# Optimization experiments

Measured on AMD Instinct MI355X. Metric: run time of the kernel, lower is better.

The kernel has to match this reference:

```python
import jax, jax.numpy as jnp
import numpy as np

# Qwen3.5-MoE Gated DeltaNet dims (from module defaults)
H = 16       # num v/k/q heads
DK = 128     # key head dim
DV = 128     # value head dim
HID = 3072   # hidden size
KD = H * DK  # key_dim = 2048
VD = H * DV  # value_dim = 2048
CONV_DIM = 2 * KD + VD  # 6144
KW = 4       # conv kernel width
EPS = 1e-6


def setup_inputs() -> dict:
    key = jax.random.key(0)
    ks = jax.random.split(key, 9)
    return {
        "hidden_states": jax.random.normal(ks[0], (2, 4096, HID), jnp.float32),
        "W_qkvz": jax.random.normal(ks[1], (HID, 2 * KD + 2 * VD), jnp.float32) * 0.02,
        "W_ba": jax.random.normal(ks[2], (HID, 2 * H), jnp.float32) * 0.02,
        "conv_w": jax.random.normal(ks[3], (CONV_DIM, KW), jnp.float32) * 0.1,
        "conv_b": jax.random.normal(ks[4], (CONV_DIM,), jnp.float32) * 0.01,
        "dt_bias": jax.random.normal(ks[5], (H,), jnp.float32) * 0.1,
        "A_log": jax.random.normal(ks[6], (H,), jnp.float32) * 0.1,
        "norm_w": jnp.ones((DV,), jnp.float32),
        "W_out": jax.random.normal(ks[7], (VD, HID), jnp.float32) * 0.02,
    }


def _l2norm(x):
    return x * jax.lax.rsqrt(jnp.sum(x * x, axis=-1, keepdims=True) + EPS)


def _gated_delta_net(hidden_states, W_qkvz, W_ba, conv_w, conv_b,
                     dt_bias, A_log, norm_w, W_out):
    B, T, _ = hidden_states.shape

    # unified qkvz projection, split [KD, KD, VD, VD]
    qkvz = hidden_states @ W_qkvz                       # [B,T,2KD+2VD]
    mixed_qkv = qkvz[..., :2 * KD + VD]                 # q|k|v  [B,T,CONV_DIM]
    z = qkvz[..., 2 * KD + VD:]                         # [B,T,VD]

    # causal depthwise conv1d over time + silu
    rhs = conv_w.T[:, None, :]                          # [KW,1,C]
    conv_out = jax.lax.conv_general_dilated(
        mixed_qkv, rhs, window_strides=(1,), padding=[(KW - 1, 0)],
        dimension_numbers=("NWC", "WIO", "NWC"),
        feature_group_count=CONV_DIM)
    mixed_qkv = jax.nn.silu(conv_out + conv_b)

    q = mixed_qkv[..., :KD].reshape(B, T, H, DK)
    k = mixed_qkv[..., KD:2 * KD].reshape(B, T, H, DK)
    v = mixed_qkv[..., 2 * KD:].reshape(B, T, H, DV)

    # beta / gate projections
    ba = hidden_states @ W_ba                           # [B,T,2H]
    beta = jax.nn.sigmoid(ba[..., :H])                  # [B,T,H]
    a = ba[..., H:]
    g = -jnp.exp(A_log) * jax.nn.softplus(a + dt_bias)  # [B,T,H] log-decay

    q = _l2norm(q) * (DK ** -0.5)
    k = _l2norm(k)

    # gated delta-rule recurrence over time (time-major scan)
    def step(S, inp):
        q_t, k_t, v_t, g_t, b_t = inp                   # [B,H,*]
        S = S * jnp.exp(g_t)[..., None, None]           # decay state [B,H,DK,DV]
        kv = jnp.einsum("bhk,bhkv->bhv", k_t, S)
        delta = (v_t - kv) * b_t[..., None]
        S = S + jnp.einsum("bhk,bhv->bhkv", k_t, delta)
        o_t = jnp.einsum("bhk,bhkv->bhv", q_t, S)
        return S, o_t

    tm = lambda x: jnp.moveaxis(x, 1, 0)                # [T,B,H,*]
    S0 = jnp.zeros((B, H, DK, DV), hidden_states.dtype)
    S_fin, o = jax.lax.scan(step, S0, (tm(q), tm(k), tm(v), tm(g), tm(beta)))
    o = jnp.moveaxis(o, 0, 1)                           # [B,T,H,DV]

    # gated RMSNorm (gate applied before norm, Mamba2/Qwen3-Next style)
    gate = jax.nn.silu(z.reshape(B, T, H, DV))
    x = o * gate
    x = x * jax.lax.rsqrt(jnp.mean(x * x, axis=-1, keepdims=True) + EPS) * norm_w

    out = x.reshape(B, T, VD) @ W_out                   # [B,T,HID]
    return out


def reference(hidden_states, W_qkvz, W_ba, conv_w, conv_b,
              dt_bias, A_log, norm_w, W_out):
    return _gated_delta_net(hidden_states, W_qkvz, W_ba, conv_w, conv_b,
                            dt_bias, A_log, norm_w, W_out)
```

## Files before the change

kernel.cpp:

```cpp
#include <hip/hip_runtime.h>
#include <cstdint>
#include <cstddef>

#define T_SEQ 4096
#define HID 3072
#define NH 16
#define DKH 128
#define KD 2048
#define VD 2048
#define N_QKVZ 8192
#define CONV_CH 6144
#define MROWS 8192

typedef unsigned short u16;
typedef unsigned int u32;

typedef __attribute__((ext_vector_type(8))) short bf16x8;
typedef __attribute__((ext_vector_type(4))) float f32x4;

__device__ __forceinline__ float bf2f(u16 u){ u32 t=((u32)u)<<16; float f; __builtin_memcpy(&f,&t,4); return f; }
__device__ __forceinline__ float bflo(u32 u){ u32 t=u<<16; float f; __builtin_memcpy(&f,&t,4); return f; }
__device__ __forceinline__ float bfhi(u32 u){ u32 t=u&0xffff0000u; float f; __builtin_memcpy(&f,&t,4); return f; }
__device__ __forceinline__ u16 f2bf(float f){ u32 i; __builtin_memcpy(&i,&f,4); return (u16)((i + 0x7fffu + ((i>>16)&1u))>>16); }

__device__ __forceinline__ void gl_lds16(const u16* g, u16* l){
    __builtin_amdgcn_global_load_lds(
        (const __attribute__((address_space(1))) void*)g,
        (__attribute__((address_space(3))) void*)l, 16, 0, 0);
}

__device__ __forceinline__ bf16x8 frag(const u16* p, int row, int stride, int k0){
    return *(const bf16x8*)(p + (size_t)row*stride + k0);
}

__global__ void k_cast(const float* __restrict__ in, u16* __restrict__ out, int n4){
    int stride = gridDim.x*blockDim.x;
    for (int i = blockIdx.x*blockDim.x + threadIdx.x; i < n4; i += stride){
        float4 v = ((const float4*)in)[i];
        u32 lo = (u32)f2bf(v.x) | ((u32)f2bf(v.y)<<16);
        u32 hi = (u32)f2bf(v.z) | ((u32)f2bf(v.w)<<16);
        ((uint2*)out)[i] = make_uint2(lo,hi);
    }
}

__global__ void k_transpose_cast(const float* __restrict__ in, u16* __restrict__ out, int R, int C){
    __shared__ u16 tile[32][33];
    int nbc = C >> 5;
    int bc = blockIdx.x % nbc, br = blockIdx.x / nbc;
    int c0 = bc<<5, r0 = br<<5;
    int tx = threadIdx.x & 31, ty = threadIdx.x >> 5;
    #pragma unroll
    for (int i=0;i<4;i++){
        int r = ty + i*8;
        tile[r][tx] = f2bf(in[(size_t)(r0+r)*C + c0 + tx]);
    }
    __syncthreads();
    #pragma unroll
    for (int i=0;i<4;i++){
        int r = ty + i*8;
        out[(size_t)(c0+r)*R + r0 + tx] = tile[tx][r];
    }
}

template<bool OUT_BF16>
__global__ __launch_bounds__(256, 2) void k_gemm_bt(const u16* __restrict__ A, const u16* __restrict__ Bt,
                                                 void* __restrict__ C1, void* __restrict__ C2,
                                                 int M, int N, int K, int csplit, int ld1, int ld2){
    __shared__ __align__(16) u16 SM[4*128*64];
    u16 (*As)[128*64] = (u16(*)[128*64])SM;
    u16 (*Bs)[128*64] = (u16(*)[128*64])(SM + 2*128*64);
    const int tid  = threadIdx.x;
    const int lane = tid & 63;
    const int wave = tid >> 6;
    const int wm = (wave >> 1) << 6;
    const int wn = (wave & 1) << 6;
    const int lr = lane & 15, lg = lane >> 4;
    const int nbn = N >> 7;
    const int per = 8*nbn;
    const int grp = blockIdx.x / per, rem = blockIdx.x % per;
    const int bm = grp*8 + (rem & 7);
    const int bn = rem >> 3;
    f32x4 acc[4][4] = {};
    const size_t aRow0 = (size_t)bm*128;
    const size_t bRow0 = (size_t)bn*128;
    const int srow = wave*32 + (lane>>3);
    const int scol = (lane&7)*8;

    auto STAGE = [&](int kt, int b){
        const u16* ga = A  + (aRow0 + srow)*K + kt + scol;
        const u16* gb = Bt + (bRow0 + srow)*K + kt + scol;
        u16* la = &As[b][wave*2048];
        u16* lb = &Bs[b][wave*2048];
        #pragma unroll
        for (int i=0;i<4;i++){
            gl_lds16(ga + (size_t)i*8*K, la + i*512);
            gl_lds16(gb + (size_t)i*8*K, lb + i*512);
        }
    };

    STAGE(0, 0);
    __syncthreads();

    const int NT = K >> 6;
    int cur = 0;
    for (int t = 0; t < NT; t++){
        if (t+1 < NT) STAGE((t+1)*64, cur^1);
        #pragma unroll
        for (int kk=0; kk<2; kk++){
            bf16x8 af[4], bfv[4];
            #pragma unroll
            for (int i=0;i<4;i++){
                af[i]  = *(const bf16x8*)&As[cur][((wm + i*16 + lr)<<6) + (kk<<5) + (lg<<3)];
                bfv[i] = *(const bf16x8*)&Bs[cur][((wn + i*16 + lr)<<6) + (kk<<5) + (lg<<3)];
            }
            __builtin_amdgcn_s_setprio(1);
            #pragma unroll
            for (int i=0;i<4;i++)
                #pragma unroll
                for (int j=0;j<4;j++)
                    acc[i][j] = __builtin_amdgcn_mfma_f32_16x16x32_bf16(af[i], bfv[j], acc[i][j], 0, 0, 0);
            __builtin_amdgcn_s_setprio(0);
        }
        __syncthreads();
        cur ^= 1;
    }

    if (OUT_BF16){
        u16* Cs = SM;
        #pragma unroll
        for (int i=0;i<4;i++)
            #pragma unroll
            for (int j=0;j<4;j++)
                #pragma unroll
                for (int r=0;r<4;r++)
                    Cs[(wm + i*16 + lg*4 + r)*136 + wn + j*16 + lr] = f2bf(acc[i][j][r]);
        __syncthreads();
        int row = tid >> 1, half = tid & 1;
        int colbase = bn*128 + half*64;
        u16* dst; int ld;
        if (bn*128 < csplit){ dst = (u16*)C1; ld = ld1; }
        else { dst = (u16*)C2; ld = ld2; colbase -= csplit; }
        u16* gp = dst + (size_t)(bm*128+row)*ld + colbase;
        const u16* sp = Cs + row*136 + half*64;
        #pragma unroll
        for (int k2=0;k2<8;k2++) *(uint4*)(gp + k2*8) = *(const uint4*)(sp + k2*8);
    } else {
        #pragma unroll
        for (int i=0;i<4;i++)
            #pragma unroll
            for (int j=0;j<4;j++)
                #pragma unroll
                for (int r=0;r<4;r++){
                    int row = bm*128 + wm + i*16 + lg*4 + r;
                    int col = bn*128 + wn + j*16 + lr;
                    ((float*)C1)[(size_t)row*ld1 + col] = acc[i][j][r];
                }
    }
}

__global__ void k_ba(const float* __restrict__ hidden, const float* __restrict__ W_ba,
                     const float* __restrict__ dt_bias, const float* __restrict__ A_log,
                     float2* __restrict__ be){
    int row = blockIdx.x*8 + (threadIdx.x>>5);
    int col = threadIdx.x & 31;
    const float* h = hidden + (size_t)row*HID;
    float s0=0.f, s1=0.f, s2=0.f, s3=0.f;
    #pragma unroll 2
    for (int k=0;k<HID;k+=4){
        s0 = fmaf(h[k],   W_ba[(k)*32+col],   s0);
        s1 = fmaf(h[k+1], W_ba[(k+1)*32+col], s1);
        s2 = fmaf(h[k+2], W_ba[(k+2)*32+col], s2);
        s3 = fmaf(h[k+3], W_ba[(k+3)*32+col], s3);
    }
    float s = (s0+s1)+(s2+s3);
    if (col < NH){
        be[(size_t)row*NH + col].x = 1.f/(1.f+expf(-s));
    } else {
        int hh = col - NH;
        float x = s + dt_bias[hh];
        float sp = fmaxf(x,0.f) + log1pf(expf(-fabsf(x)));
        be[(size_t)row*NH + hh].y = -expf(A_log[hh])*sp;
    }
}

__global__ __launch_bounds__(256) void k_conv_silu(const u16* __restrict__ qkv, const float* __restrict__ conv_w,
                            const float* __restrict__ conv_b, u16* __restrict__ mixed){
    __shared__ float hsum[4][8];
    const int bid = blockIdx.x, tid = threadIdx.x;
    const int c0 = (bid % 24) << 8;
    const long bt0 = (long)(bid / 24) * 8;
    const int ts0 = (int)(bt0 % T_SEQ);
    const int c = c0 + tid;
    const u16* in = qkv + (size_t)bt0*CONV_CH + c;
    float4 w = *(const float4*)(conv_w + c*4);
    float bias = conv_b[c];
    float w0=0.f, w1=0.f, w2=0.f;
    if (ts0 > 0){
        w0 = bf2f(in[-3*CONV_CH]); w1 = bf2f(in[-2*CONV_CH]); w2 = bf2f(in[-1*CONV_CH]);
    }
    float sv[8];
    #pragma unroll
    for (int j=0;j<8;j++){
        float xc = bf2f(in[(ptrdiff_t)j*CONV_CH]);
        float acc = bias + w.x*w0 + w.y*w1 + w.z*w2 + w.w*xc;
        sv[j] = acc / (1.f + __expf(-acc));
        w0 = w1; w1 = w2; w2 = xc;
    }
    if (c0 < 2*KD){
        float ss[8];
        #pragma unroll
        for (int j=0;j<8;j++) ss[j] = sv[j]*sv[j];
        #pragma unroll
        for (int m=1;m<64;m<<=1)
            #pragma unroll
            for (int j=0;j<8;j++) ss[j] += __shfl_xor(ss[j], m, 64);
        if ((tid&63)==0)
            #pragma unroll
            for (int j=0;j<8;j++) hsum[tid>>6][j] = ss[j];
        __syncthreads();
        int head = tid>>7;
        float qs = (c0 + head*128 < KD) ? 0.08838834764831845f : 1.f;
        #pragma unroll
        for (int j=0;j<8;j++){
            float tot = hsum[head*2][j] + hsum[head*2+1][j];
            sv[j] *= rsqrtf(tot + 1e-6f) * qs;
        }
    }
    u16* outp = mixed + (size_t)bt0*CONV_CH + c;
    #pragma unroll
    for (int j=0;j<8;j++) outp[(size_t)j*CONV_CH] = f2bf(sv[j]);
}

__global__ __launch_bounds__(512) void k_prep(const u16* __restrict__ mixed,
        const float2* __restrict__ be, u16* __restrict__ Wcg, u16* __restrict__ Ucg,
        float* __restrict__ barr){
    __shared__ __align__(16) u16 Ks[64*128];
    __shared__ __align__(16) u16 Vs[64*128];
    __shared__ float Am[64*64];
    __shared__ __align__(16) float RHS[64*256];
    __shared__ float bv[64], betav[64], lamv[64];
    const int tid = threadIdx.x;
    const int lane = tid & 63, wave = tid >> 6;
    const int lr = lane & 15, lg = lane >> 4;
    const int chunk = blockIdx.x;
    const int ci = chunk & 63, bh = chunk >> 6, b = bh >> 4, h = bh & 15;
    const size_t rowbase = (size_t)b*T_SEQ + ci*64;

    const u16* kg = mixed + rowbase*CONV_CH + KD + h*128;
    const u16* vg = mixed + rowbase*CONV_CH + 2*KD + h*128;
    #pragma unroll
    for (int pass=0; pass<2; pass++){
        int row = (tid>>4) + pass*32;
        int co = (tid&15)*8;
        gl_lds16(kg + (size_t)row*CONV_CH + co, Ks + row*128 + co);
        gl_lds16(vg + (size_t)row*CONV_CH + co, Vs + row*128 + co);
    }
    if (tid < 64){
        float2 bg = be[(rowbase + tid)*NH + h];
        float acc = bg.y;
        #pragma unroll
        for (int m=1;m<64;m<<=1){ float u = __shfl_up(acc, m, 64); if (tid >= m) acc += u; }
        bv[tid] = acc; betav[tid] = bg.x; lamv[tid] = __expf(acc);
        barr[(size_t)chunk*64 + tid] = acc;
    }
    __syncthreads();
    #pragma unroll
    for (int i=0;i<2;i++){
        int tile = wave*2 + i;
        int tm = tile>>2, tn = tile&3;
        f32x4 acc = {};
        #pragma unroll
        for (int kk=0;kk<4;kk++)
            acc = __builtin_amdgcn_mfma_f32_16x16x32_bf16(
                frag(Ks, tm*16+lr, 128, kk*32+lg*8),
                frag(Ks, tn*16+lr, 128, kk*32+lg*8), acc, 0,0,0);
        #pragma unroll
        for (int r=0;r<4;r++){
            int t = tm*16 + lg*4 + r, s = tn*16 + lr;
            Am[t*64+s] = (t>s) ? betav[t]*__expf(bv[t]-bv[s])*acc[r] : 0.f;
        }
    }
    __syncthreads();
    for (int i=tid; i<64*256; i+=512){
        int r = i>>8, j = i&255;
        RHS[i] = (j<128) ? betav[r]*lamv[r]*bf2f(Ks[r*128+j])
                         : betav[r]*bf2f(Vs[r*128 + (j-128)]);
    }
    __syncthreads();
    for (int blk=0; blk<8; blk++){
        int base = blk*8;
        if (base){
            int r = base + (tid>>6);
            int j0 = (tid&63)*4;
            float4 x = *(float4*)&RHS[r*256 + j0];
            for (int s=0; s<base; s++){
                float a = Am[r*64+s];
                float4 y = *(float4*)&RHS[s*256 + j0];
                x.x = fmaf(-a, y.x, x.x); x.y = fmaf(-a, y.y, x.y);
                x.z = fmaf(-a, y.z, x.z); x.w = fmaf(-a, y.w, x.w);
            }
            *(float4*)&RHS[r*256 + j0] = x;
        }
        __syncthreads();
        if (tid < 256){
            float x[8];
            #pragma unroll
            for (int i=0;i<8;i++) x[i] = RHS[(base+i)*256 + tid];
            #pragma unroll
            for (int r=1;r<8;r++)
                #pragma unroll
                for (int s=0;s<r;s++)
                    x[r] = fmaf(-Am[(base+r)*64 + base+s], x[s], x[r]);
            #pragma unroll
            for (int i=1;i<8;i++) RHS[(base+i)*256 + tid] = x[i];
        }
        __syncthreads();
    }
    for (int i=tid; i<8192; i+=512){
        int r = i>>7, c = i&127;
        Wcg[(size_t)chunk*8192 + i] = f2bf(RHS[r*256 + c]);
        Ucg[(size_t)chunk*8192 + i] = f2bf(RHS[r*256 + 128 + c]);
    }
}

__global__ __launch_bounds__(256) void k_seq(const u16* __restrict__ mixed,
        const u16* __restrict__ Wcg, const u16* __restrict__ Ucg,
        const float* __restrict__ barr,
        float* __restrict__ o1g, u16* __restrict__ DTg){
    __shared__ __align__(16) u16 WcS[2][64*128];
    __shared__ __align__(16) u16 Ks[2][64*128];
    __shared__ __align__(16) u16 Qs[2][64*128];
    __shared__ __align__(16) u16 UcS[2][64*32];
    __shared__ __align__(16) u16 KpT[128*72];
    __shared__ __align__(16) u16 DT[32*72];
    __shared__ __align__(16) u16 STh[32*136];
    __shared__ __align__(16) u16 STl[32*136];
    __shared__ float bvv[2][64], esc[64];
    const int tid = threadIdx.x, lane = tid&63, wave = tid>>6;
    const int lr = lane&15, lg = lane>>4;
    const int blk = blockIdx.x;
    const int bh = blk & 31, vs = blk >> 5;
    const int b = bh>>4, h = bh&15, v0 = vs*32;
    const u16* qgb = mixed + (size_t)b*T_SEQ*CONV_CH + h*128;
    const u16* kgb = qgb + KD;
    const int urow = tid>>2, uc8 = (tid&3)*8;

    float sreg[4][4];
    #pragma unroll
    for (int i=0;i<4;i++)
        #pragma unroll
        for (int r=0;r<4;r++) sreg[i][r] = 0.f;
    for (int i=tid; i<32*136; i+=256){ STh[i]=0; STl[i]=0; }

    auto STAGE = [&](int ci2, int bf){
        const size_t ch = (size_t)(bh*64 + ci2);
        #pragma unroll
        for (int pass=0; pass<4; pass++){
            gl_lds16(Wcg + ch*8192 + pass*2048 + tid*8, &WcS[bf][pass*2048 + tid*8]);
            int row = pass*16 + (tid>>4), co = (tid&15)*8;
            gl_lds16(kgb + ((size_t)(ci2*64) + row)*CONV_CH + co, &Ks[bf][row*128 + co]);
            gl_lds16(qgb + ((size_t)(ci2*64) + row)*CONV_CH + co, &Qs[bf][row*128 + co]);
        }
    };

    STAGE(0, 0);
    *(uint4*)&UcS[0][urow*32 + uc8] = *(const uint4*)(Ucg + (size_t)(bh*64)*8192 + urow*128 + v0 + uc8);
    if (tid<64) bvv[0][tid] = barr[(size_t)(bh*64)*64 + tid];
    __syncthreads();

    for (int ci=0; ci<64; ci++){
        const int cur = ci&1, nxt = cur^1;
        const size_t chunk = (size_t)(bh*64 + ci);
        const size_t rowbase = (size_t)b*T_SEQ + ci*64;
        uint4 ucv = {0,0,0,0}; float bvn = 0.f;
        const bool havenext = (ci+1 < 64);
        if (havenext){
            STAGE(ci+1, nxt);
            ucv = *(const uint4*)(Ucg + (chunk+1)*8192 + urow*128 + v0 + uc8);
            if (tid<64) bvn = barr[(chunk+1)*64 + tid];
        }
        if (tid<64) esc[tid] = __expf(bvv[cur][63] - bvv[cur][tid]);
        #pragma unroll
        for (int i=0;i<2;i++){
            int tile = wave*2 + i, tm = tile>>1, tn = tile&1;
            f32x4 acc = {};
            #pragma unroll
            for (int kk=0;kk<4;kk++){
                bf16x8 af = frag(WcS[cur], tm*16+lr, 128, kk*32+lg*8);
                acc = __builtin_amdgcn_mfma_f32_16x16x32_bf16(af, frag(STh, tn*16+lr, 136, kk*32+lg*8), acc, 0,0,0);
                acc = __builtin_amdgcn_mfma_f32_16x16x32_bf16(af, frag(STl, tn*16+lr, 136, kk*32+lg*8), acc, 0,0,0);
            }
            #pragma unroll
            for (int r=0;r<4;r++){
                int t = tm*16+lg*4+r, vv = tn*16+lr;
                DT[vv*72 + t] = f2bf(bf2f(UcS[cur][t*32+vv]) - acc[r]);
            }
        }
        #pragma unroll
        for (int i=0;i<2;i++){
            int tile = wave*2 + i, tm = tile>>1, tn = tile&1;
            f32x4 acc = {};
            #pragma unroll
            for (int kk=0;kk<4;kk++){
                bf16x8 af = frag(Qs[cur], tm*16+lr, 128, kk*32+lg*8);
                acc = __builtin_amdgcn_mfma_f32_16x16x32_bf16(af, frag(STh, tn*16+lr, 136, kk*32+lg*8), acc, 0,0,0);
                acc = __builtin_amdgcn_mfma_f32_16x16x32_bf16(af, frag(STl, tn*16+lr, 136, kk*32+lg*8), acc, 0,0,0);
            }
            #pragma unroll
            for (int r=0;r<4;r++){
                int t = tm*16+lg*4+r, vv = tn*16+lr;
                o1g[((rowbase + t)*NH + h)*DKH + v0 + vv] = acc[r]*__expf(bvv[cur][t]);
            }
        }
        __syncthreads();
        for (int i=tid; i<8192; i+=256){
            int t = i>>7, k = i&127;
            KpT[(size_t)k*72 + t] = f2bf(bf2f(Ks[cur][t*128 + k]) * esc[t]);
        }
        { int vv = tid>>3, c = (tid&7)*8;
          *(uint4*)(DTg + chunk*8192 + (size_t)(v0+vv)*64 + c) = *(const uint4*)&DT[vv*72 + c]; }
        if (havenext){
            *(uint4*)&UcS[nxt][urow*32 + uc8] = ucv;
            if (tid<64) bvv[nxt][tid] = bvn;
        }
        __syncthreads();
        float lamC = __expf(bvv[cur][63]);
        #pragma unroll
        for (int i=0;i<4;i++){
            int tile = wave*4 + i, tm = tile>>1, tn = tile&1;
            f32x4 acc;
            #pragma unroll
            for (int r=0;r<4;r++) acc[r] = lamC * sreg[i][r];
            #pragma unroll
            for (int kk=0;kk<2;kk++)
                acc = __builtin_amdgcn_mfma_f32_16x16x32_bf16(
                    frag(KpT, tm*16+lr, 72, kk*32+lg*8),
                    frag(DT,  tn*16+lr, 72, kk*32+lg*8), acc, 0,0,0);
            #pragma unroll
            for (int r=0;r<4;r++){
                int k = tm*16+lg*4+r, vv = tn*16+lr;
                sreg[i][r] = acc[r];
                u16 hi = f2bf(acc[r]);
                STh[vv*136 + k] = hi;
                STl[vv*136 + k] = f2bf(acc[r] - bf2f(hi));
            }
        }
        __syncthreads();
    }
}

__global__ __launch_bounds__(256) void k_out(const u16* __restrict__ mixed,
        const float* __restrict__ barr, const float* __restrict__ o1g,
        const u16* __restrict__ DTg, float* __restrict__ o){
    __shared__ __align__(16) u16 Qs[64*128];
    __shared__ __align__(16) u16 Ks[64*128];
    __shared__ __align__(16) u16 DTs[128*64];
    __shared__ __align__(16) u16 QKm[64*72];
    __shared__ float bvv[64];
    const int tid = threadIdx.x, lane = tid&63, wave = tid>>6;
    const int lr = lane&15, lg = lane>>4;
    const int chunk = blockIdx.x;
    const int ci = chunk&63, bh = chunk>>6, b = bh>>4, h = bh&15;
    const size_t rowbase = (size_t)b*T_SEQ + ci*64;
    const u16* qg = mixed + rowbase*CONV_CH + h*128;
    const u16* kg = qg + KD;
    #pragma unroll
    for (int pass=0; pass<4; pass++){
        int row = pass*16 + (tid>>4), co = (tid&15)*8;
        gl_lds16(qg + (size_t)row*CONV_CH + co, Qs + row*128 + co);
        gl_lds16(kg + (size_t)row*CONV_CH + co, Ks + row*128 + co);
        gl_lds16(DTg + (size_t)chunk*8192 + pass*2048 + tid*8, DTs + pass*2048 + tid*8);
    }
    if (tid<64) bvv[tid] = barr[(size_t)chunk*64 + tid];
    __syncthreads();
    {
        f32x4 acc[4];
        #pragma unroll
        for (int tn=0; tn<4; tn++){
            f32x4 a = {};
            #pragma unroll
            for (int kk=0;kk<4;kk++)
                a = __builtin_amdgcn_mfma_f32_16x16x32_bf16(
                    frag(Qs, wave*16+lr, 128, kk*32+lg*8),
                    frag(Ks, tn*16+lr, 128, kk*32+lg*8), a, 0,0,0);
            acc[tn] = a;
        }
        #pragma unroll
        for (int tn=0;tn<4;tn++)
            #pragma unroll
            for (int r=0;r<4;r++){
                int t = wave*16+lg*4+r, s = tn*16+lr;
                float val = (t>=s) ? acc[tn][r]*__expf(bvv[t]-bvv[s]) : 0.f;
                QKm[t*72+s] = f2bf(val);
            }
    }
    __syncthreads();
    f32x4 acc[8] = {};
    #pragma unroll
    for (int kk=0;kk<2;kk++){
        bf16x8 af = frag(QKm, wave*16+lr, 72, kk*32+lg*8);
        #pragma unroll
        for (int tn=0;tn<8;tn++)
            acc[tn] = __builtin_amdgcn_mfma_f32_16x16x32_bf16(af, frag(DTs, tn*16+lr, 64, kk*32+lg*8), acc[tn], 0,0,0);
    }
    #pragma unroll
    for (int tn=0;tn<8;tn++)
        #pragma unroll
        for (int r=0;r<4;r++){
            int t = wave*16+lg*4+r, v = tn*16+lr;
            size_t idx = ((rowbase + t)*NH + h)*DKH + v;
            o[idx] = o1g[idx] + acc[tn][r];
        }
}

__global__ void k_gatenorm(const float* __restrict__ o, const u16* __restrict__ zbuf,
                           const float* __restrict__ norm_w, u16* __restrict__ x){
    int gw   = blockIdx.x*4 + (threadIdx.x>>6);
    int lane = threadIdx.x & 63;
    int bt = gw >> 4, h = gw & 15;
    const float* opr = o + ((size_t)bt*NH + h)*DKH + lane*2;
    const u16* zp = zbuf + (size_t)bt*VD + h*DKH + lane*2;
    float o0 = opr[0], o1 = opr[1];
    u32 zu = *(const u32*)zp;
    float z0 = bflo(zu), z1 = bfhi(zu);
    float x0 = o0 * (z0/(1.f+__expf(-z0)));
    float x1 = o1 * (z1/(1.f+__expf(-z1)));
    float ss = x0*x0 + x1*x1;
    #pragma unroll
    for (int m=1;m<64;m<<=1) ss += __shfl_xor(ss, m, 64);
    float sc = rsqrtf(ss*(1.f/128.f) + 1e-6f);
    x0 *= sc*norm_w[lane*2]; x1 *= sc*norm_w[lane*2+1];
    ((u32*)x)[(size_t)bt*(VD/2) + h*(DKH/2) + lane] = (u32)f2bf(x0) | ((u32)f2bf(x1)<<16);
}

extern "C" void kernel_launch(void* const* d_in, const int* in_sizes, int n_in,
                              void* d_out, int out_size, void* d_ws, size_t ws_size,
                              hipStream_t stream){
    (void)in_sizes; (void)n_in; (void)out_size; (void)ws_size;
    const float* hidden = (const float*)d_in[0];
    const float* W_qkvz = (const float*)d_in[1];
    const float* W_ba   = (const float*)d_in[2];
    const float* conv_w = (const float*)d_in[3];
    const float* conv_b = (const float*)d_in[4];
    const float* dt_bias= (const float*)d_in[5];
    const float* A_log  = (const float*)d_in[6];
    const float* norm_w = (const float*)d_in[7];
    const float* W_out  = (const float*)d_in[8];
    float* out = (float*)d_out;

    char* ws = (char*)d_ws;
    size_t off = 0;
    auto alloc = [&](size_t bytes)->char*{ char* p = ws + off; off += (bytes + 255) & ~(size_t)255; return p; };
    char* poolA = alloc(100663296);
    u16*   h_bf = (u16*)poolA;
    u16*   WqT  = (u16*)(poolA + 50331648);
    u16*   Wcg  = (u16*)poolA;
    u16*   Ucg  = (u16*)(poolA + 33554432);
    u16*   DTg  = (u16*)(poolA + 67108864);
    float* o_b  = (float*)poolA;
    char* poolB = alloc(100663296);
    u16*   qkv_lin = (u16*)poolB;
    float* o1g  = (float*)poolB;
    float* barr = (float*)(poolB + 67108864);
    u16*   x_b  = (u16*)poolB;
    u16*   WoT  = (u16*)  alloc((size_t)HID*VD*2);
    u16*   zbuf = (u16*)  alloc((size_t)MROWS*VD*2);
    u16*   mixed= (u16*)  alloc((size_t)MROWS*CONV_CH*2);
    float2* be_b= (float2*)alloc((size_t)MROWS*NH*8);

    k_cast<<<2048,256,0,stream>>>(hidden, h_bf, MROWS*HID/4);
    k_transpose_cast<<<(HID/32)*(N_QKVZ/32),256,0,stream>>>(W_qkvz, WqT, HID, N_QKVZ);
    k_transpose_cast<<<(VD/32)*(HID/32),256,0,stream>>>(W_out, WoT, VD, HID);
    k_gemm_bt<true><<<(MROWS/128)*(N_QKVZ/128),256,0,stream>>>(h_bf, WqT, qkv_lin, zbuf,
                         MROWS, N_QKVZ, HID, CONV_CH, CONV_CH, VD);
    k_ba<<<MROWS/8,256,0,stream>>>(hidden, W_ba, dt_bias, A_log, be_b);
    k_conv_silu<<<(MROWS/8)*24,256,0,stream>>>(qkv_lin, conv_w, conv_b, mixed);
    k_prep<<<2048,512,0,stream>>>(mixed, be_b, Wcg, Ucg, barr);
    k_seq<<<128,256,0,stream>>>(mixed, Wcg, Ucg, barr, o1g, DTg);
    k_out<<<2048,256,0,stream>>>(mixed, barr, o1g, DTg, o_b);
    k_gatenorm<<<MROWS*NH/4,256,0,stream>>>(o_b, zbuf, norm_w, x_b);
    k_gemm_bt<false><<<(MROWS/128)*(HID/128),256,0,stream>>>(x_b, WoT, out, nullptr,
                         MROWS, HID, VD, 1<<30, HID, 0);
}
```

Baseline: 1.384 ms.

## Enlarge GEMM block tile to 256x128 with triple-buffered LDS pipeline

Replaces the double-buffered 128x128 GEMM with a 512-thread kernel that computes 256x128 tiles. It keeps three LDS stages in flight, with explicit vmcnt waits and raw s_barriers, so global loads run two k-steps ahead of the MFMA work. The aim is to hide more global-load latency and get more reuse per B tile for both projection GEMMs. The cost is much larger LDS use, about 147KB, which leaves only one block per CU, and the hand-tuned waitcnt logic is fragile.

```diff
diff --git a/kernel.cpp b/kernel.cpp
--- a/kernel.cpp
+++ b/kernel.cpp
@@ -63,17 +63,16 @@
 }
 
 template<bool OUT_BF16>
-__global__ __launch_bounds__(256, 2) void k_gemm_bt(const u16* __restrict__ A, const u16* __restrict__ Bt,
+__global__ __launch_bounds__(512, 2) void k_gemm3(const u16* __restrict__ A, const u16* __restrict__ Bt,
                                                  void* __restrict__ C1, void* __restrict__ C2,
                                                  int M, int N, int K, int csplit, int ld1, int ld2){
-    __shared__ __align__(16) u16 SM[4*128*64];
-    u16 (*As)[128*64] = (u16(*)[128*64])SM;
-    u16 (*Bs)[128*64] = (u16(*)[128*64])(SM + 2*128*64);
+    __shared__ __align__(16) u16 AsB[3*256*64];
+    __shared__ __align__(16) u16 BsB[3*128*64];
     const int tid  = threadIdx.x;
     const int lane = tid & 63;
     const int wave = tid >> 6;
-    const int wm = (wave >> 1) << 6;
-    const int wn = (wave & 1) << 6;
+    const int wm = wave >> 1;
+    const int wn = wave & 1;
     const int lr = lane & 15, lg = lane >> 4;
     const int nbn = N >> 7;
     const int per = 8*nbn;
@@ -81,37 +80,48 @@
     const int bm = grp*8 + (rem & 7);
     const int bn = rem >> 3;
     f32x4 acc[4][4] = {};
-    const size_t aRow0 = (size_t)bm*128;
+    const size_t aRow0 = (size_t)bm*256;
     const size_t bRow0 = (size_t)bn*128;
-    const int srow = wave*32 + (lane>>3);
-    const int scol = (lane&7)*8;
-
-    auto STAGE = [&](int kt, int b){
-        const u16* ga = A  + (aRow0 + srow)*K + kt + scol;
-        const u16* gb = Bt + (bRow0 + srow)*K + kt + scol;
-        u16* la = &As[b][wave*2048];
-        u16* lb = &Bs[b][wave*2048];
-        #pragma unroll
-        for (int i=0;i<4;i++){
-            gl_lds16(ga + (size_t)i*8*K, la + i*512);
-            gl_lds16(gb + (size_t)i*8*K, lb + i*512);
-        }
+    const int srow = tid >> 3;
+    const int scol = (tid & 7) * 8;
+
+    auto STAGE = [&](int t, int slot){
+        const u16* ga = A  + (aRow0 + srow)*K + t*64 + scol;
+        const u16* gb = Bt + (bRow0 + srow)*K + t*64 + scol;
+        u16* la = AsB + slot*(256*64) + tid*8;
+        u16* lb = BsB + slot*(128*64) + tid*8;
+        #pragma unroll
+        for (int j=0;j<4;j++) gl_lds16(ga + (size_t)(j*64)*K, la + j*4096);
+        #pragma unroll
+        for (int j=0;j<2;j++) gl_lds16(gb + (size_t)(j*64)*K, lb + j*4096);
     };
 
+    const int NT = K >> 6;
     STAGE(0, 0);
-    __syncthreads();
-
-    const int NT = K >> 6;
-    int cur = 0;
-    for (int t = 0; t < NT; t++){
-        if (t+1 < NT) STAGE((t+1)*64, cur^1);
+    if (NT > 1) STAGE(1, 1);
+
+    for (int t=0; t<NT; t++){
+        const int slot = t % 3;
+        if (t+2 < NT){
+            STAGE(t+2, (t+2)%3);
+            asm volatile("s_waitcnt vmcnt(12)" ::: "memory");
+        } else if (t+1 < NT){
+            asm volatile("s_waitcnt vmcnt(6)" ::: "memory");
+        } else {
+            asm volatile("s_waitcnt vmcnt(0)" ::: "memory");
+        }
+        __builtin_amdgcn_sched_barrier(0);
+        __builtin_amdgcn_s_barrier();
+        __builtin_amdgcn_sched_barrier(0);
+        const u16* Asl = AsB + slot*(256*64);
+        const u16* Bsl = BsB + slot*(128*64);
         #pragma unroll
         for (int kk=0; kk<2; kk++){
             bf16x8 af[4], bfv[4];
             #pragma unroll
             for (int i=0;i<4;i++){
-                af[i]  = *(const bf16x8*)&As[cur][((wm + i*16 + lr)<<6) + (kk<<5) + (lg<<3)];
-                bfv[i] = *(const bf16x8*)&Bs[cur][((wn + i*16 + lr)<<6) + (kk<<5) + (lg<<3)];
+                af[i]  = frag(Asl, wm*64 + i*16 + lr, 64, kk*32 + lg*8);
+                bfv[i] = frag(Bsl, wn*64 + i*16 + lr, 64, kk*32 + lg*8);
             }
             __builtin_amdgcn_s_setprio(1);
             #pragma unroll
@@ -121,26 +131,28 @@
                     acc[i][j] = __builtin_amdgcn_mfma_f32_16x16x32_bf16(af[i], bfv[j], acc[i][j], 0, 0, 0);
             __builtin_amdgcn_s_setprio(0);
         }
-        __syncthreads();
-        cur ^= 1;
+        asm volatile("s_waitcnt lgkmcnt(0)" ::: "memory");
+        __builtin_amdgcn_sched_barrier(0);
+        __builtin_amdgcn_s_barrier();
+        __builtin_amdgcn_sched_barrier(0);
     }
 
     if (OUT_BF16){
-        u16* Cs = SM;
+        u16* Cs = AsB;
         #pragma unroll
         for (int i=0;i<4;i++)
             #pragma unroll
             for (int j=0;j<4;j++)
                 #pragma unroll
                 for (int r=0;r<4;r++)
-                    Cs[(wm + i*16 + lg*4 + r)*136 + wn + j*16 + lr] = f2bf(acc[i][j][r]);
+                    Cs[(wm*64 + i*16 + lg*4 + r)*136 + wn*64 + j*16 + lr] = f2bf(acc[i][j][r]);
         __syncthreads();
         int row = tid >> 1, half = tid & 1;
         int colbase = bn*128 + half*64;
         u16* dst; int ld;
         if (bn*128 < csplit){ dst = (u16*)C1; ld = ld1; }
         else { dst = (u16*)C2; ld = ld2; colbase -= csplit; }
-        u16* gp = dst + (size_t)(bm*128+row)*ld + colbase;
+        u16* gp = dst + (size_t)(bm*256+row)*ld + colbase;
         const u16* sp = Cs + row*136 + half*64;
         #pragma unroll
         for (int k2=0;k2<8;k2++) *(uint4*)(gp + k2*8) = *(const uint4*)(sp + k2*8);
@@ -151,8 +163,8 @@
             for (int j=0;j<4;j++)
                 #pragma unroll
                 for (int r=0;r<4;r++){
-                    int row = bm*128 + wm + i*16 + lg*4 + r;
-                    int col = bn*128 + wn + j*16 + lr;
+                    int row = bm*256 + wm*64 + i*16 + lg*4 + r;
+                    int col = bn*128 + wn*64 + j*16 + lr;
                     ((float*)C1)[(size_t)row*ld1 + col] = acc[i][j][r];
                 }
     }
@@ -571,7 +583,7 @@
     k_cast<<<2048,256,0,stream>>>(hidden, h_bf, MROWS*HID/4);
     k_transpose_cast<<<(HID/32)*(N_QKVZ/32),256,0,stream>>>(W_qkvz, WqT, HID, N_QKVZ);
     k_transpose_cast<<<(VD/32)*(HID/32),256,0,stream>>>(W_out, WoT, VD, HID);
-    k_gemm_bt<true><<<(MROWS/128)*(N_QKVZ/128),256,0,stream>>>(h_bf, WqT, qkv_lin, zbuf,
+    k_gemm3<true><<<(MROWS/256)*(N_QKVZ/128),512,0,stream>>>(h_bf, WqT, qkv_lin, zbuf,
                          MROWS, N_QKVZ, HID, CONV_CH, CONV_CH, VD);
     k_ba<<<MROWS/8,256,0,stream>>>(hidden, W_ba, dt_bias, A_log, be_b);
     k_conv_silu<<<(MROWS/8)*24,256,0,stream>>>(qkv_lin, conv_w, conv_b, mixed);
@@ -579,6 +591,6 @@
     k_seq<<<128,256,0,stream>>>(mixed, Wcg, Ucg, barr, o1g, DTg);
     k_out<<<2048,256,0,stream>>>(mixed, barr, o1g, DTg, o_b);
     k_gatenorm<<<MROWS*NH/4,256,0,stream>>>(o_b, zbuf, norm_w, x_b);
-    k_gemm_bt<false><<<(MROWS/128)*(HID/128),256,0,stream>>>(x_b, WoT, out, nullptr,
+    k_gemm3<false><<<(MROWS/256)*(HID/128),512,0,stream>>>(x_b, WoT, out, nullptr,
                          MROWS, HID, VD, 1<<30, HID, 0);
 }
```

After: 1.658 ms. 1.2x slower.
